# Kernel tuning notes

Measured on AMD Instinct MI355X. Metric: run time of the kernel, lower is better.

## Reference

```python
import jax, jax.numpy as jnp
import numpy as np

N_NODES = 10000
N_EDGES = 160000
FEAT = 32
EMB = 32
VOCAB = 32000
EDGE_DIM = 9
HID = 32  # edge MLP hidden


def setup_inputs() -> dict:
    key = jax.random.key(0)
    ks = jax.random.split(key, 16)
    s = lambda *sh: 1.0 / np.sqrt(sh[0])
    inp = {
        "signal": jax.random.randint(ks[0], (1,), 0, VOCAB, dtype=jnp.int64) if jax.config.jax_enable_x64 else jax.random.randint(ks[0], (1,), 0, VOCAB).astype(jnp.int32),
        "x": jax.random.normal(ks[1], (N_NODES, FEAT), dtype=jnp.float32),
        "edge_index": jax.random.randint(ks[2], (2, N_EDGES), 0, N_NODES).astype(jnp.int32),
        "edge_attr": jax.random.normal(ks[3], (N_EDGES, EDGE_DIM), dtype=jnp.float32),
        # edge MLP 1: 9 -> 32 -> FEAT*EMB
        "w1a": jax.random.normal(ks[4], (EDGE_DIM, HID), dtype=jnp.float32) * s(EDGE_DIM),
        "b1a": jnp.zeros((HID,), jnp.float32),
        "w1b": jax.random.normal(ks[5], (HID, FEAT * EMB), dtype=jnp.float32) * s(HID),
        "b1b": jnp.zeros((FEAT * EMB,), jnp.float32),
        "root1": jax.random.normal(ks[6], (FEAT, EMB), dtype=jnp.float32) * s(FEAT),
        "bias1": jnp.zeros((EMB,), jnp.float32),
        # edge MLP 2: 9 -> 32 -> EMB*EMB
        "w2a": jax.random.normal(ks[7], (EDGE_DIM, HID), dtype=jnp.float32) * s(EDGE_DIM),
        "b2a": jnp.zeros((HID,), jnp.float32),
        "w2b": jax.random.normal(ks[8], (HID, EMB * EMB), dtype=jnp.float32) * s(HID),
        "b2b": jnp.zeros((EMB * EMB,), jnp.float32),
        "root2": jax.random.normal(ks[9], (EMB, EMB), dtype=jnp.float32) * s(EMB),
        "bias2": jnp.zeros((EMB,), jnp.float32),
        "emb_table": jax.random.normal(ks[10], (VOCAB, EMB), dtype=jnp.float32),
    }
    return inp


def nnconv(x, edge_index, edge_attr, wa, ba, wb, bb, root, bias, in_ch, out_ch):
    # edge MLP -> per-edge weight matrices [E, in_ch, out_ch]
    h = jax.nn.relu(edge_attr @ wa + ba)
    W_e = (h @ wb + bb).reshape(-1, in_ch, out_ch)
    src, dst = edge_index[0], edge_index[1]
    # gather source node features, per-edge matmul
    msg = jnp.einsum("ei,eio->eo", x[src], W_e)  # [E, out_ch]
    summed = jax.ops.segment_sum(msg, dst, num_segments=N_NODES)
    cnt = jax.ops.segment_sum(jnp.ones((msg.shape[0],), msg.dtype), dst, num_segments=N_NODES)
    aggr = summed / jnp.maximum(cnt, 1.0)[:, None]  # scatter-mean (0 for isolated nodes)
    return aggr + x @ root + bias


def reference(signal, x, edge_index, edge_attr,
              w1a, b1a, w1b, b1b, root1, bias1,
              w2a, b2a, w2b, b2b, root2, bias2, emb_table):
    h = jax.nn.relu(nnconv(x, edge_index, edge_attr, w1a, b1a, w1b, b1b, root1, bias1, FEAT, EMB))
    h = jax.nn.relu(nnconv(h, edge_index, edge_attr, w2a, b2a, w2b, b2b, root2, bias2, EMB, EMB))
    sig = emb_table[signal]          # [1, EMB]
    sig = sig[0]                      # squeeze leading 1 (matches torch branch)
    scores = h @ sig                  # [N]
    return jax.nn.log_softmax(scores, axis=0)
```

## Files before the change

kernel.cpp:

```cpp
#include <hip/hip_runtime.h>
#include <math.h>

#define NN 10000
#define NE 160000
#define C  32
#define ED 9
#define EAP 12

typedef __attribute__((ext_vector_type(8))) short short8v;
typedef __attribute__((ext_vector_type(4))) float float4v;

__device__ inline unsigned short f2bf(float f) {
    unsigned int u = __float_as_uint(f);
    return (unsigned short)((u + 0x7fffu + ((u >> 16) & 1u)) >> 16);
}

__global__ __launch_bounds__(256) void zfill_kernel(uint4* __restrict__ p, int n16) {
    const int i = blockIdx.x * 256 + threadIdx.x;
    if (i < n16) p[i] = uint4{0u, 0u, 0u, 0u};
}

__global__ __launch_bounds__(256) void hist_kernel(const int* __restrict__ ei,
                                                   int* __restrict__ cnt_src,
                                                   int* __restrict__ cnt_dst) {
    const int e = blockIdx.x * 256 + threadIdx.x;
    if (e < NE) {
        atomicAdd(&cnt_src[ei[e]], 1);
        atomicAdd(&cnt_dst[ei[NE + e]], 1);
    }
}

__global__ __launch_bounds__(1024) void scan_kernel(const int* __restrict__ cnt,
                                                    int* __restrict__ offs) {
    __shared__ int part[1024];
    const int t = threadIdx.x;
    const int base = t * 10;
    int loc[10];
    int s = 0;
#pragma unroll
    for (int j = 0; j < 10; ++j) {
        int v = (base + j < NN) ? cnt[base + j] : 0;
        loc[j] = s;
        s += v;
    }
    part[t] = s;
    __syncthreads();
    for (int off = 1; off < 1024; off <<= 1) {
        int v = (t >= off) ? part[t - off] : 0;
        __syncthreads();
        part[t] += v;
        __syncthreads();
    }
    const int excl = (t == 0) ? 0 : part[t - 1];
#pragma unroll
    for (int j = 0; j < 10; ++j)
        if (base + j < NN) offs[base + j] = excl + loc[j];
    if (t == 1023) offs[NN] = part[1023];
}

__global__ __launch_bounds__(256) void scatter_kernel(const int* __restrict__ ei,
                                                      const float* __restrict__ ea,
                                                      const int* __restrict__ offs,
                                                      int* __restrict__ cursor,
                                                      int* __restrict__ dst_s,
                                                      float* __restrict__ ea_s) {
    const int e = blockIdx.x * 256 + threadIdx.x;
    if (e < NE) {
        const int b   = ei[e];
        const int pos = offs[b] + atomicAdd(&cursor[b], 1);
        dst_s[pos] = ei[NE + e];
#pragma unroll
        for (int j = 0; j < ED; ++j)
            ea_s[(size_t)pos * EAP + j] = ea[(size_t)e * ED + j];
    }
}

__global__ __launch_bounds__(256) void wbt_kernel(const float* __restrict__ wb,
                                                  float* __restrict__ wbT) {
    const int idx = blockIdx.x * 256 + threadIdx.x;
    const int i = idx & 31, k = (idx >> 5) & 31, o = idx >> 10;
    wbT[idx] = wb[k * (C * C) + i * C + o];
}

__global__ __launch_bounds__(256) void u_gemm2(const float* __restrict__ xin,
                                               const float* __restrict__ wbT,
                                               const float* __restrict__ bb,
                                               unsigned short* __restrict__ UT,
                                               float* __restrict__ xb) {
    __shared__ float xs[16 * C];
    const int b   = blockIdx.x;
    const int nb  = (b >> 2) * 16;
    const int o0  = (b & 3) * 8;
    const int tid = threadIdx.x;
    for (int t = tid; t < 16 * C; t += 256) xs[t] = xin[nb * C + t];
    __syncthreads();

    const int op = tid >> 5, k = tid & 31, o = o0 + op;
    float4v wv[8];
    const float* wp = wbT + ((size_t)o * C + k) * C;
#pragma unroll
    for (int i4 = 0; i4 < 8; ++i4)
        wv[i4] = *reinterpret_cast<const float4v*>(wp + i4 * 4);

#pragma unroll
    for (int n = 0; n < 16; ++n) {
        float acc = 0.f;
#pragma unroll
        for (int i4 = 0; i4 < 8; ++i4) {
            const float4v xv = *reinterpret_cast<const float4v*>(&xs[n * C + i4 * 4]);
            acc += xv.x * wv[i4].x + xv.y * wv[i4].y + xv.z * wv[i4].z + xv.w * wv[i4].w;
        }
        UT[(size_t)(nb + n) * (C * C) + o * C + k] = f2bf(acc);
    }
    if (o0 == 0) {
#pragma unroll
        for (int t = 0; t < 2; ++t) {
            const int idx = t * 256 + tid;
            const int n = idx >> 5, oo = idx & 31;
            float acc = 0.f;
#pragma unroll
            for (int i = 0; i < C; ++i) acc += xs[n * C + i] * bb[i * C + oo];
            xb[(nb + n) * C + oo] = acc;
        }
    }
}

__global__ __launch_bounds__(256) void edge4_kernel(const int* __restrict__ offs,
                                                    const int* __restrict__ dst_s,
                                                    const float* __restrict__ ea_s,
                                                    const float* __restrict__ wa,
                                                    const float* __restrict__ ba,
                                                    const unsigned short* __restrict__ UT,
                                                    const float* __restrict__ xb,
                                                    float* __restrict__ sumbuf) {
    __shared__ float was[ED * C];
    __shared__ float bas[C];
    const int tid = threadIdx.x;
    for (int t = tid; t < ED * C; t += 256) was[t] = wa[t];
    if (tid < C) bas[tid] = ba[tid];
    __syncthreads();

    const int w  = tid >> 6;
    const int l  = tid & 63;
    const int s  = blockIdx.x * 4 + w;
    const int q  = l >> 4;
    const int el = l & 15;

    const int e0 = offs[s], e1 = offs[s + 1];
    if (e0 == e1) return;

    const unsigned short* up = UT + (size_t)s * (C * C);
    const short8v B1 = *reinterpret_cast<const short8v*>(up + el * C + q * 8);
    const short8v B2 = *reinterpret_cast<const short8v*>(up + (el + 16) * C + q * 8);
    const float c1 = xb[s * C + el];
    const float c2 = xb[s * C + el + 16];
    const float4v C1 = {c1, c1, c1, c1};
    const float4v C2 = {c2, c2, c2, c2};
    float hb[8];
#pragma unroll
    for (int i = 0; i < 8; ++i) hb[i] = bas[q * 8 + i];

    for (int pb = e0; pb < e1; pb += 16) {
        const int p  = pb + el;
        const int pc = (p < e1) ? p : e0;
        const float* eap = ea_s + (size_t)pc * EAP;
        const float4v ea0 = *reinterpret_cast<const float4v*>(eap);
        const float4v ea1 = *reinterpret_cast<const float4v*>(eap + 4);
        const float   ea8 = eap[8];

        float h[8];
#pragma unroll
        for (int i = 0; i < 8; ++i) h[i] = hb[i];
#pragma unroll
        for (int j = 0; j < ED; ++j) {
            const float ev = (j == 0) ? ea0.x : (j == 1) ? ea0.y : (j == 2) ? ea0.z
                           : (j == 3) ? ea0.w : (j == 4) ? ea1.x : (j == 5) ? ea1.y
                           : (j == 6) ? ea1.z : (j == 7) ? ea1.w : ea8;
            const float4v w0 = *reinterpret_cast<const float4v*>(&was[j * C + q * 8]);
            const float4v w1 = *reinterpret_cast<const float4v*>(&was[j * C + q * 8 + 4]);
            h[0] += ev * w0.x; h[1] += ev * w0.y; h[2] += ev * w0.z; h[3] += ev * w0.w;
            h[4] += ev * w1.x; h[5] += ev * w1.y; h[6] += ev * w1.z; h[7] += ev * w1.w;
        }
        union { int u[4]; short8v v; } A;
#pragma unroll
        for (int v = 0; v < 4; ++v) {
            const unsigned lo = f2bf(fmaxf(h[2 * v], 0.f));
            const unsigned hi = f2bf(fmaxf(h[2 * v + 1], 0.f));
            A.u[v] = (int)(lo | (hi << 16));
        }
        const float4v d1 = __builtin_amdgcn_mfma_f32_16x16x32_bf16(A.v, B1, C1, 0, 0, 0);
        const float4v d2 = __builtin_amdgcn_mfma_f32_16x16x32_bf16(A.v, B2, C2, 0, 0, 0);
#pragma unroll
        for (int r = 0; r < 4; ++r) {
            const int pe = pb + q * 4 + r;
            if (pe < e1) {
                const int dst = dst_s[pe];
                atomicAdd(&sumbuf[(size_t)dst * C + el],      d1[r]);
                atomicAdd(&sumbuf[(size_t)dst * C + el + 16], d2[r]);
            }
        }
    }
}

__global__ __launch_bounds__(256) void node_kernel(const float* __restrict__ xin,
                                                   const float* __restrict__ sumbuf,
                                                   const int* __restrict__ cnt,
                                                   const float* __restrict__ root,
                                                   const float* __restrict__ bias,
                                                   float* __restrict__ outb) {
    __shared__ float rs[C * C];
    __shared__ float bs[C];
    __shared__ float xs[8][C];
    const int tid = threadIdx.x;
    for (int t = tid; t < C * C; t += 256) rs[t] = root[t];
    if (tid < C) bs[tid] = bias[tid];
    const int nl = tid >> 5, o = tid & 31;
    const int n  = blockIdx.x * 8 + nl;
    xs[nl][o] = (n < NN) ? xin[n * C + o] : 0.f;
    __syncthreads();
    if (n < NN) {
        float acc = bs[o];
#pragma unroll
        for (int i = 0; i < C; ++i) acc += xs[nl][i] * rs[i * C + o];
        const float cn = fmaxf((float)cnt[n], 1.f);
        acc += sumbuf[n * C + o] / cn;
        outb[n * C + o] = fmaxf(acc, 0.f);
    }
}

__global__ __launch_bounds__(256) void score_kernel(const float* __restrict__ h,
                                                    const float* __restrict__ emb,
                                                    const int* __restrict__ signal,
                                                    float* __restrict__ scores) {
    __shared__ float sig[C];
    if (threadIdx.x < C) sig[threadIdx.x] = emb[(size_t)signal[0] * C + threadIdx.x];
    __syncthreads();
    const int n = blockIdx.x * 256 + threadIdx.x;
    if (n < NN) {
        float acc = 0.f;
#pragma unroll
        for (int o = 0; o < C; ++o) acc += h[n * C + o] * sig[o];
        scores[n] = acc;
    }
}

__global__ __launch_bounds__(1024) void reduce_kernel(const float* __restrict__ scores,
                                                      float* __restrict__ red) {
    __shared__ float sm[16];
    __shared__ float ss[16];
    const int tid = threadIdx.x;
    float m = -INFINITY;
    for (int n = tid; n < NN; n += 1024) m = fmaxf(m, scores[n]);
    for (int off = 32; off; off >>= 1) m = fmaxf(m, __shfl_down(m, off, 64));
    if ((tid & 63) == 0) sm[tid >> 6] = m;
    __syncthreads();
    if (tid == 0) {
        float mm = sm[0];
        for (int w = 1; w < 16; ++w) mm = fmaxf(mm, sm[w]);
        sm[0] = mm;
    }
    __syncthreads();
    const float gmax = sm[0];
    float s = 0.f;
    for (int n = tid; n < NN; n += 1024) s += expf(scores[n] - gmax);
    for (int off = 32; off; off >>= 1) s += __shfl_down(s, off, 64);
    if ((tid & 63) == 0) ss[tid >> 6] = s;
    __syncthreads();
    if (tid == 0) {
        float t = 0.f;
        for (int w = 0; w < 16; ++w) t += ss[w];
        red[0] = gmax;
        red[1] = logf(t);
    }
}

__global__ __launch_bounds__(256) void out_kernel(const float* __restrict__ scores,
                                                  const float* __restrict__ red,
                                                  float* __restrict__ out) {
    const int n = blockIdx.x * 256 + threadIdx.x;
    if (n < NN) out[n] = scores[n] - red[0] - red[1];
}

extern "C" void kernel_launch(void* const* d_in, const int* in_sizes, int n_in,
                              void* d_out, int out_size, void* d_ws, size_t ws_size,
                              hipStream_t stream) {
    const int*   signal = (const int*)d_in[0];
    const float* x      = (const float*)d_in[1];
    const int*   ei     = (const int*)d_in[2];
    const float* ea     = (const float*)d_in[3];
    const float* w1a    = (const float*)d_in[4];
    const float* b1a    = (const float*)d_in[5];
    const float* w1b    = (const float*)d_in[6];
    const float* b1b    = (const float*)d_in[7];
    const float* root1  = (const float*)d_in[8];
    const float* bias1  = (const float*)d_in[9];
    const float* w2a    = (const float*)d_in[10];
    const float* b2a    = (const float*)d_in[11];
    const float* w2b    = (const float*)d_in[12];
    const float* b2b    = (const float*)d_in[13];
    const float* root2  = (const float*)d_in[14];
    const float* bias2  = (const float*)d_in[15];
    const float* emb    = (const float*)d_in[16];

    float* ws = (float*)d_ws;
    unsigned short* UT = (unsigned short*)ws;
    float* xb      = ws + 5120000;
    float* h1      = xb + NN * C;
    float* h2      = h1 + NN * C;
    float* ea_s    = h2 + NN * C;
    float* wbT1    = ea_s + (size_t)NE * EAP;
    float* wbT2    = wbT1 + 32768;
    float* scores  = wbT2 + 32768;
    float* red     = scores + NN;
    float* sumbuf1 = red + 16;
    float* sumbuf2 = sumbuf1 + NN * C;
    int*   cnt_src = (int*)(sumbuf2 + NN * C);
    int*   cnt_dst = cnt_src + NN;
    int*   cursor  = cnt_dst + NN;
    int*   offs    = cursor + NN;
    int*   dst_s   = offs + NN + 16;

    const int n16 = 167500;
    zfill_kernel<<<(n16 + 255) / 256, 256, 0, stream>>>((uint4*)sumbuf1, n16);

    hist_kernel<<<(NE + 255) / 256, 256, 0, stream>>>(ei, cnt_src, cnt_dst);
    scan_kernel<<<1, 1024, 0, stream>>>(cnt_src, offs);
    scatter_kernel<<<(NE + 255) / 256, 256, 0, stream>>>(ei, ea, offs, cursor, dst_s, ea_s);
    wbt_kernel<<<128, 256, 0, stream>>>(w1b, wbT1);
    wbt_kernel<<<128, 256, 0, stream>>>(w2b, wbT2);

    u_gemm2<<<2500, 256, 0, stream>>>(x, wbT1, b1b, UT, xb);
    edge4_kernel<<<2500, 256, 0, stream>>>(offs, dst_s, ea_s, w1a, b1a, UT, xb, sumbuf1);
    node_kernel<<<NN / 8, 256, 0, stream>>>(x, sumbuf1, cnt_dst, root1, bias1, h1);

    u_gemm2<<<2500, 256, 0, stream>>>(h1, wbT2, b2b, UT, xb);
    edge4_kernel<<<2500, 256, 0, stream>>>(offs, dst_s, ea_s, w2a, b2a, UT, xb, sumbuf2);
    node_kernel<<<NN / 8, 256, 0, stream>>>(h1, sumbuf2, cnt_dst, root2, bias2, h2);

    score_kernel<<<(NN + 255) / 256, 256, 0, stream>>>(h2, emb, signal, scores);
    reduce_kernel<<<1, 1024, 0, stream>>>(scores, red);
    out_kernel<<<(NN + 255) / 256, 256, 0, stream>>>(scores, red, (float*)d_out);
}
```

Measured before the change: 178.9 us.

## Fuse node updates into GEMM/score kernels and merge small launches

Result: faster. 161.1 us (-10.0%).

```diff
diff --git a/kernel.cpp b/kernel.cpp
--- a/kernel.cpp
+++ b/kernel.cpp
@@ -15,9 +15,25 @@
     return (unsigned short)((u + 0x7fffu + ((u >> 16) & 1u)) >> 16);
 }
 
-__global__ __launch_bounds__(256) void zfill_kernel(uint4* __restrict__ p, int n16) {
-    const int i = blockIdx.x * 256 + threadIdx.x;
-    if (i < n16) p[i] = uint4{0u, 0u, 0u, 0u};
+#define ZB 655
+__global__ __launch_bounds__(256) void prep_kernel(uint4* __restrict__ zreg, int n16,
+                                                   const float* __restrict__ w1b,
+                                                   const float* __restrict__ w2b,
+                                                   float* __restrict__ wbT1,
+                                                   float* __restrict__ wbT2) {
+    const int b = blockIdx.x, tid = threadIdx.x;
+    if (b < ZB) {
+        const int i = b * 256 + tid;
+        if (i < n16) zreg[i] = uint4{0u, 0u, 0u, 0u};
+    } else if (b < ZB + 128) {
+        const int idx = (b - ZB) * 256 + tid;
+        const int i = idx & 31, k = (idx >> 5) & 31, o = idx >> 10;
+        wbT1[idx] = w1b[k * (C * C) + i * C + o];
+    } else {
+        const int idx = (b - ZB - 128) * 256 + tid;
+        const int i = idx & 31, k = (idx >> 5) & 31, o = idx >> 10;
+        wbT2[idx] = w2b[k * (C * C) + i * C + o];
+    }
 }
 
 __global__ __launch_bounds__(256) void hist_kernel(const int* __restrict__ ei,
@@ -32,8 +48,9 @@
 
 __global__ __launch_bounds__(1024) void scan_kernel(const int* __restrict__ cnt,
                                                     int* __restrict__ offs) {
-    __shared__ int part[1024];
+    __shared__ int wtot[16];
     const int t = threadIdx.x;
+    const int lane = t & 63, wid = t >> 6;
     const int base = t * 10;
     int loc[10];
     int s = 0;
@@ -43,19 +60,27 @@
         loc[j] = s;
         s += v;
     }
-    part[t] = s;
-    __syncthreads();
-    for (int off = 1; off < 1024; off <<= 1) {
-        int v = (t >= off) ? part[t - off] : 0;
-        __syncthreads();
-        part[t] += v;
-        __syncthreads();
-    }
-    const int excl = (t == 0) ? 0 : part[t - 1];
+    int inc = s;
+    for (int d = 1; d < 64; d <<= 1) {
+        int v = __shfl_up(inc, d, 64);
+        if (lane >= d) inc += v;
+    }
+    if (lane == 63) wtot[wid] = inc;
+    __syncthreads();
+    if (t < 16) {
+        int w = wtot[t];
+        for (int d = 1; d < 16; d <<= 1) {
+            int v = __shfl_up(w, d, 64);
+            if (t >= d) w += v;
+        }
+        wtot[t] = w;
+    }
+    __syncthreads();
+    const int excl = inc - s + (wid ? wtot[wid - 1] : 0);
 #pragma unroll
     for (int j = 0; j < 10; ++j)
         if (base + j < NN) offs[base + j] = excl + loc[j];
-    if (t == 1023) offs[NN] = part[1023];
+    if (t == 1023) offs[NN] = wtot[15];
 }
 
 __global__ __launch_bounds__(256) void scatter_kernel(const int* __restrict__ ei,
@@ -75,13 +100,6 @@
     }
 }
 
-__global__ __launch_bounds__(256) void wbt_kernel(const float* __restrict__ wb,
-                                                  float* __restrict__ wbT) {
-    const int idx = blockIdx.x * 256 + threadIdx.x;
-    const int i = idx & 31, k = (idx >> 5) & 31, o = idx >> 10;
-    wbT[idx] = wb[k * (C * C) + i * C + o];
-}
-
 __global__ __launch_bounds__(256) void u_gemm2(const float* __restrict__ xin,
                                                const float* __restrict__ wbT,
                                                const float* __restrict__ bb,
@@ -121,6 +139,70 @@
 #pragma unroll
             for (int i = 0; i < C; ++i) acc += xs[n * C + i] * bb[i * C + oo];
             xb[(nb + n) * C + oo] = acc;
+        }
+    }
+}
+
+__global__ __launch_bounds__(256) void u_gemm2_fused(const float* __restrict__ xin,
+                                                     const float* __restrict__ sumbuf1,
+                                                     const int* __restrict__ cnt,
+                                                     const float* __restrict__ root1,
+                                                     const float* __restrict__ bias1,
+                                                     const float* __restrict__ wbT,
+                                                     const float* __restrict__ bb,
+                                                     unsigned short* __restrict__ UT,
+                                                     float* __restrict__ xb,
+                                                     float* __restrict__ h1out) {
+    __shared__ float xs[16 * C];
+    __shared__ float hs[16 * C];
+    const int b   = blockIdx.x;
+    const int nb  = (b >> 2) * 16;
+    const int o0  = (b & 3) * 8;
+    const int tid = threadIdx.x;
+    for (int t = tid; t < 16 * C; t += 256) xs[t] = xin[nb * C + t];
+    __syncthreads();
+
+#pragma unroll
+    for (int t = 0; t < 2; ++t) {
+        const int idx = t * 256 + tid;
+        const int n = idx >> 5, oo = idx & 31;
+        float acc = bias1[oo];
+#pragma unroll
+        for (int i = 0; i < C; ++i) acc += xs[n * C + i] * root1[i * C + oo];
+        const float cn = fmaxf((float)cnt[nb + n], 1.f);
+        acc += sumbuf1[(size_t)(nb + n) * C + oo] / cn;
+        const float h = fmaxf(acc, 0.f);
+        hs[n * C + oo] = h;
+        if (o0 == 0) h1out[(size_t)(nb + n) * C + oo] = h;
+    }
+    __syncthreads();
+
+    const int op = tid >> 5, k = tid & 31, o = o0 + op;
+    float4v wv[8];
+    const float* wp = wbT + ((size_t)o * C + k) * C;
+#pragma unroll
+    for (int i4 = 0; i4 < 8; ++i4)
+        wv[i4] = *reinterpret_cast<const float4v*>(wp + i4 * 4);
+
+#pragma unroll
+    for (int n = 0; n < 16; ++n) {
+        float acc = 0.f;
+#pragma unroll
+        for (int i4 = 0; i4 < 8; ++i4) {
+            const float4v xv = *reinterpret_cast<const float4v*>(&hs[n * C + i4 * 4]);
+            acc += xv.x * wv[i4].x + xv.y * wv[i4].y + xv.z * wv[i4].z + xv.w * wv[i4].w;
+        }
+        UT[(size_t)(nb + n) * (C * C) + o * C + k] = f2bf(acc);
+    }
+    if (o0 == 0) {
+#pragma unroll
+        for (int t = 0; t < 2; ++t) {
+            const int idx = t * 256 + tid;
+            const int n = idx >> 5, oo = idx & 31;
+            float acc = 0.f;
+#pragma unroll
+            for (int i = 0; i < C; ++i) acc += hs[n * C + i] * bb[i * C + oo];
+            xb[(size_t)(nb + n) * C + oo] = acc;
         }
     }
 }
@@ -202,50 +284,41 @@
     }
 }
 
-__global__ __launch_bounds__(256) void node_kernel(const float* __restrict__ xin,
+__global__ __launch_bounds__(256) void node2_score(const float* __restrict__ h1,
                                                    const float* __restrict__ sumbuf,
                                                    const int* __restrict__ cnt,
                                                    const float* __restrict__ root,
                                                    const float* __restrict__ bias,
-                                                   float* __restrict__ outb) {
+                                                   const float* __restrict__ emb,
+                                                   const int* __restrict__ signal,
+                                                   float* __restrict__ scores) {
     __shared__ float rs[C * C];
     __shared__ float bs[C];
+    __shared__ float sig[C];
     __shared__ float xs[8][C];
     const int tid = threadIdx.x;
     for (int t = tid; t < C * C; t += 256) rs[t] = root[t];
-    if (tid < C) bs[tid] = bias[tid];
+    if (tid < C) {
+        bs[tid]  = bias[tid];
+        sig[tid] = emb[(size_t)signal[0] * C + tid];
+    }
     const int nl = tid >> 5, o = tid & 31;
     const int n  = blockIdx.x * 8 + nl;
-    xs[nl][o] = (n < NN) ? xin[n * C + o] : 0.f;
-    __syncthreads();
-    if (n < NN) {
-        float acc = bs[o];
-#pragma unroll
-        for (int i = 0; i < C; ++i) acc += xs[nl][i] * rs[i * C + o];
-        const float cn = fmaxf((float)cnt[n], 1.f);
-        acc += sumbuf[n * C + o] / cn;
-        outb[n * C + o] = fmaxf(acc, 0.f);
-    }
-}
-
-__global__ __launch_bounds__(256) void score_kernel(const float* __restrict__ h,
-                                                    const float* __restrict__ emb,
-                                                    const int* __restrict__ signal,
-                                                    float* __restrict__ scores) {
-    __shared__ float sig[C];
-    if (threadIdx.x < C) sig[threadIdx.x] = emb[(size_t)signal[0] * C + threadIdx.x];
-    __syncthreads();
-    const int n = blockIdx.x * 256 + threadIdx.x;
-    if (n < NN) {
-        float acc = 0.f;
-#pragma unroll
-        for (int o = 0; o < C; ++o) acc += h[n * C + o] * sig[o];
-        scores[n] = acc;
-    }
-}
-
-__global__ __launch_bounds__(1024) void reduce_kernel(const float* __restrict__ scores,
-                                                      float* __restrict__ red) {
+    xs[nl][o] = h1[(size_t)n * C + o];
+    __syncthreads();
+    float acc = bs[o];
+#pragma unroll
+    for (int i = 0; i < C; ++i) acc += xs[nl][i] * rs[i * C + o];
+    const float cn = fmaxf((float)cnt[n], 1.f);
+    acc += sumbuf[(size_t)n * C + o] / cn;
+    float val = fmaxf(acc, 0.f) * sig[o];
+#pragma unroll
+    for (int off = 16; off; off >>= 1) val += __shfl_xor(val, off, 32);
+    if (o == 0) scores[n] = val;
+}
+
+__global__ __launch_bounds__(1024) void reduce_out_kernel(const float* __restrict__ scores,
+                                                          float* __restrict__ out) {
     __shared__ float sm[16];
     __shared__ float ss[16];
     const int tid = threadIdx.x;
@@ -269,16 +342,11 @@
     if (tid == 0) {
         float t = 0.f;
         for (int w = 0; w < 16; ++w) t += ss[w];
-        red[0] = gmax;
-        red[1] = logf(t);
-    }
-}
-
-__global__ __launch_bounds__(256) void out_kernel(const float* __restrict__ scores,
-                                                  const float* __restrict__ red,
-                                                  float* __restrict__ out) {
-    const int n = blockIdx.x * 256 + threadIdx.x;
-    if (n < NN) out[n] = scores[n] - red[0] - red[1];
+        ss[0] = logf(t);
+    }
+    __syncthreads();
+    const float sub = gmax + ss[0];
+    for (int n = tid; n < NN; n += 1024) out[n] = scores[n] - sub;
 }
 
 extern "C" void kernel_launch(void* const* d_in, const int* in_sizes, int n_in,
@@ -306,13 +374,11 @@
     unsigned short* UT = (unsigned short*)ws;
     float* xb      = ws + 5120000;
     float* h1      = xb + NN * C;
-    float* h2      = h1 + NN * C;
-    float* ea_s    = h2 + NN * C;
+    float* ea_s    = h1 + NN * C;
     float* wbT1    = ea_s + (size_t)NE * EAP;
     float* wbT2    = wbT1 + 32768;
     float* scores  = wbT2 + 32768;
-    float* red     = scores + NN;
-    float* sumbuf1 = red + 16;
+    float* sumbuf1 = scores + NN;
     float* sumbuf2 = sumbuf1 + NN * C;
     int*   cnt_src = (int*)(sumbuf2 + NN * C);
     int*   cnt_dst = cnt_src + NN;
@@ -321,23 +387,17 @@
     int*   dst_s   = offs + NN + 16;
 
     const int n16 = 167500;
-    zfill_kernel<<<(n16 + 255) / 256, 256, 0, stream>>>((uint4*)sumbuf1, n16);
-
+
+    prep_kernel<<<ZB + 256, 256, 0, stream>>>((uint4*)sumbuf1, n16, w1b, w2b, wbT1, wbT2);
     hist_kernel<<<(NE + 255) / 256, 256, 0, stream>>>(ei, cnt_src, cnt_dst);
     scan_kernel<<<1, 1024, 0, stream>>>(cnt_src, offs);
     scatter_kernel<<<(NE + 255) / 256, 256, 0, stream>>>(ei, ea, offs, cursor, dst_s, ea_s);
-    wbt_kernel<<<128, 256, 0, stream>>>(w1b, wbT1);
-    wbt_kernel<<<128, 256, 0, stream>>>(w2b, wbT2);
-
     u_gemm2<<<2500, 256, 0, stream>>>(x, wbT1, b1b, UT, xb);
     edge4_kernel<<<2500, 256, 0, stream>>>(offs, dst_s, ea_s, w1a, b1a, UT, xb, sumbuf1);
-    node_kernel<<<NN / 8, 256, 0, stream>>>(x, sumbuf1, cnt_dst, root1, bias1, h1);
-
-    u_gemm2<<<2500, 256, 0, stream>>>(h1, wbT2, b2b, UT, xb);
+    u_gemm2_fused<<<2500, 256, 0, stream>>>(x, sumbuf1, cnt_dst, root1, bias1,
+                                            wbT2, b2b, UT, xb, h1);
     edge4_kernel<<<2500, 256, 0, stream>>>(offs, dst_s, ea_s, w2a, b2a, UT, xb, sumbuf2);
-    node_kernel<<<NN / 8, 256, 0, stream>>>(h1, sumbuf2, cnt_dst, root2, bias2, h2);
-
-    score_kernel<<<(NN + 255) / 256, 256, 0, stream>>>(h2, emb, signal, scores);
-    reduce_kernel<<<1, 1024, 0, stream>>>(scores, red);
-    out_kernel<<<(NN + 255) / 256, 256, 0, stream>>>(scores, red, (float*)d_out);
-}
+    node2_score<<<1250, 256, 0, stream>>>(h1, sumbuf2, cnt_dst, root2, bias2,
+                                          emb, signal, scores);
+    reduce_out_kernel<<<1, 1024, 0, stream>>>(scores, (float*)d_out);
+}
```
